# Kernel tuning notes

Measured on AMD Instinct MI355X. Metric: run time of the kernel, lower is better.

The kernel has to match this reference:

```python
import jax, jax.numpy as jnp
import numpy as np

N_NODES = 100000
N_EDGES = 1600000
VOCAB = 50000
F_DIM = 128
N_GRAPHS = 64
N_LABELS = 20


def setup_inputs() -> dict:
    key = jax.random.key(0)
    ks = jax.random.split(key, 12)
    s = 1.0 / np.sqrt(F_DIM)
    inp = {
        "x": jax.random.randint(ks[0], (N_NODES,), 0, VOCAB),
        "edge_index": jax.random.randint(ks[1], (2, N_EDGES), 0, N_NODES),
        "batch": jnp.sort(jax.random.randint(ks[2], (N_NODES,), 0, N_GRAPHS)),
        "emb": jax.random.normal(ks[3], (VOCAB, F_DIM), jnp.float32),
        "w1_rel": jax.random.normal(ks[4], (F_DIM, F_DIM), jnp.float32) * s,
        "w1_root": jax.random.normal(ks[5], (F_DIM, F_DIM), jnp.float32) * s,
        "b1": jnp.zeros((F_DIM,), jnp.float32),
        "w2_rel": jax.random.normal(ks[6], (F_DIM, F_DIM), jnp.float32) * s,
        "w2_root": jax.random.normal(ks[7], (F_DIM, F_DIM), jnp.float32) * s,
        "b2": jnp.zeros((F_DIM,), jnp.float32),
        "lw1": jax.random.normal(ks[8], (2 * F_DIM, 128), jnp.float32) * (1.0 / np.sqrt(2 * F_DIM)),
        "lb1": jnp.zeros((128,), jnp.float32),
        "lw2": jax.random.normal(ks[9], (128, 64), jnp.float32) * (1.0 / np.sqrt(128)),
        "lb2": jnp.zeros((64,), jnp.float32),
        "lw3": jax.random.normal(ks[10], (64, N_LABELS), jnp.float32) * (1.0 / np.sqrt(64)),
        "lb3": jnp.zeros((N_LABELS,), jnp.float32),
    }
    return inp


def graph_conv(h, src, dst, w_rel, w_root, b):
    # PyG GraphConv (aggr='add'): out_i = W_rel @ sum_{j->i} h_j + b + W_root @ h_i
    agg = jax.ops.segment_sum(h[src], dst, num_segments=N_NODES)  # [N, F]
    return agg @ w_rel + b + h @ w_root


def reference(x, edge_index, batch, emb, w1_rel, w1_root, b1,
              w2_rel, w2_root, b2, lw1, lb1, lw2, lb2, lw3, lb3):
    src, dst = edge_index[0], edge_index[1]
    h = emb[x]                                              # [N, F]
    h = jax.nn.relu(graph_conv(h, src, dst, w1_rel, w1_root, b1))
    h = jax.nn.relu(graph_conv(h, src, dst, w2_rel, w2_root, b2))
    # global max pool + global mean pool per graph
    gmax = jax.ops.segment_max(h, batch, num_segments=N_GRAPHS)  # [G, F]
    gsum = jax.ops.segment_sum(h, batch, num_segments=N_GRAPHS)
    counts = jax.ops.segment_sum(jnp.ones((N_NODES,), h.dtype), batch,
                                 num_segments=N_GRAPHS)
    gmean = gsum / jnp.maximum(counts, 1.0)[:, None]
    g = jnp.concatenate([gmax, gmean], axis=1)              # [G, 2F]
    g = jax.nn.relu(g @ lw1 + lb1)
    g = jax.nn.relu(g @ lw2 + lb2)
    # NOTE: original applies log_softmax over dim=0 (the graph dim) - kept faithful
    return jax.nn.log_softmax(g @ lw3 + lb3, axis=0)
```

## Files before the change

### kernel.cpp

```cpp
#include <hip/hip_runtime.h>
#include <hip/hip_bf16.h>

#define N_NODES   100000
#define N_EDGES   1600000
#define N_GRAPHS  64
#define FDIM      128
#define N_LABELS  20
#define NBK       64
#define P_BKT     1563
#define NCHUNKS   64
#define CHUNK     25000
#define SCAN_M    (P_BKT * NCHUNKS)
#define SB_BLOCKS 391
#define APITCH    40
#define PCHUNKS   32

typedef __bf16 bf16x8 __attribute__((ext_vector_type(8)));
typedef float  f32x4  __attribute__((ext_vector_type(4)));
union frag_u { uint4 u; bf16x8 b; };

__device__ __forceinline__ unsigned bfr(float v) {
  unsigned b = __float_as_uint(v);
  return (b + 0x7fffu + ((b >> 16) & 1u)) >> 16;
}

__global__ __launch_bounds__(256) void init_kernel(
    float* __restrict__ pool, float* __restrict__ zrow,
    int* __restrict__ csr, int* __restrict__ csr2, int* __restrict__ offsets) {
  int i = blockIdx.x * 256 + threadIdx.x;
  if (i < N_GRAPHS * 256) pool[i] = 0.f;
  if (i < FDIM) zrow[i] = 0.f;
  if (i < 8) { csr[N_EDGES + i] = 0; csr2[N_EDGES + i] = 0; }
  if (i == 8) offsets[N_NODES] = N_EDGES;
}

__global__ __launch_bounds__(256) void cvt_emb_kernel(
    const float* __restrict__ emb, unsigned short* __restrict__ embbf) {
  int i = blockIdx.x * 256 + threadIdx.x;
  float4 v = ((const float4*)emb)[i];
  uint2 o;
  o.x = bfr(v.x) | (bfr(v.y) << 16);
  o.y = bfr(v.z) | (bfr(v.w) << 16);
  ((uint2*)embbf)[i] = o;
}

__global__ __launch_bounds__(256) void cvt_w_kernel(
    const float* __restrict__ w1rel, const float* __restrict__ w1rt,
    const float* __restrict__ w2rel, const float* __restrict__ w2rt,
    unsigned short* __restrict__ wt1, unsigned short* __restrict__ wt2) {
  int gid = blockIdx.x * 256 + threadIdx.x;
  int l = gid >> 15;
  int rem = gid & 32767;
  int c = rem >> 8, k = rem & 255;
  const float* w = l ? ((k < 128) ? w2rel : w2rt) : ((k < 128) ? w1rel : w1rt);
  float v = w[(size_t)(k & 127) * FDIM + c];
  (l ? wt2 : wt1)[c * 256 + k] = (unsigned short)bfr(v);
}

__global__ __launch_bounds__(256) void histA_kernel(
    const int* __restrict__ ei, int* __restrict__ cntmat) {
  __shared__ int hist[P_BKT];
  int tid = threadIdx.x;
  for (int i = tid; i < P_BKT; i += 256) hist[i] = 0;
  __syncthreads();
  int base = blockIdx.x * CHUNK;
  for (int i = tid; i < CHUNK; i += 256) {
    int d = ei[N_EDGES + base + i];
    atomicAdd(&hist[d >> 6], 1);
  }
  __syncthreads();
  for (int p = tid; p < P_BKT; p += 256)
    cntmat[p * NCHUNKS + blockIdx.x] = hist[p];
}

__global__ __launch_bounds__(256) void scanB1_kernel(
    const int* __restrict__ v, int* __restrict__ part,
    int* __restrict__ bsum) {
  __shared__ int s[256];
  int tid = threadIdx.x;
  int i = blockIdx.x * 256 + tid;
  int val = (i < SCAN_M) ? v[i] : 0;
  s[tid] = val;
  __syncthreads();
  for (int off = 1; off < 256; off <<= 1) {
    int t = (tid >= off) ? s[tid - off] : 0;
    __syncthreads();
    s[tid] += t;
    __syncthreads();
  }
  if (i < SCAN_M) part[i] = s[tid] - val;
  if (tid == 255) bsum[blockIdx.x] = s[255];
}

__global__ __launch_bounds__(512) void scanB2_kernel(int* __restrict__ bsum) {
  __shared__ int s[512];
  int tid = threadIdx.x;
  int v = (tid < SB_BLOCKS) ? bsum[tid] : 0;
  s[tid] = v;
  __syncthreads();
  for (int off = 1; off < 512; off <<= 1) {
    int t = (tid >= off) ? s[tid - off] : 0;
    __syncthreads();
    s[tid] += t;
    __syncthreads();
  }
  if (tid < SB_BLOCKS) bsum[tid] = s[tid] - v;
}

__global__ __launch_bounds__(256) void scanB3_kernel(
    int* __restrict__ part, const int* __restrict__ bsum,
    int* __restrict__ bstart) {
  int i = blockIdx.x * 256 + threadIdx.x;
  if (i < SCAN_M) {
    int o = part[i] + bsum[blockIdx.x];
    part[i] = o;
    if ((i & (NCHUNKS - 1)) == 0) bstart[i >> 6] = o;
  }
  if (blockIdx.x == 0 && threadIdx.x == 0) bstart[P_BKT] = N_EDGES;
}

__global__ __launch_bounds__(256) void scatA_kernel(
    const int* __restrict__ ei, const int* __restrict__ S,
    int* __restrict__ ebuf) {
  __shared__ int rc[P_BKT];
  int tid = threadIdx.x;
  for (int p = tid; p < P_BKT; p += 256)
    rc[p] = S[p * NCHUNKS + blockIdx.x];
  __syncthreads();
  int base = blockIdx.x * CHUNK;
  for (int i = tid; i < CHUNK; i += 256) {
    int s0 = ei[base + i];
    int d0 = ei[N_EDGES + base + i];
    int pos = atomicAdd(&rc[d0 >> 6], 1);
    ebuf[pos] = (s0 << 6) | (d0 & 63);
  }
}

__global__ __launch_bounds__(256) void fill2_kernel(
    const int* __restrict__ ebuf, const int* __restrict__ bstart,
    const int* __restrict__ x, int* __restrict__ offsets,
    int* __restrict__ csr, int* __restrict__ csr2) {
  __shared__ int ldeg[NBK], loffs[NBK], rc2[NBK];
  int tid = threadIdx.x;
  int p = blockIdx.x;
  int beg = bstart[p], end = bstart[p + 1];
  if (tid < NBK) ldeg[tid] = 0;
  __syncthreads();
  for (int i = beg + tid; i < end; i += 256)
    atomicAdd(&ldeg[ebuf[i] & 63], 1);
  __syncthreads();
  if (tid == 0) {
    int run = 0;
    for (int r = 0; r < NBK; ++r) { loffs[r] = run; run += ldeg[r]; }
  }
  __syncthreads();
  if (tid < NBK) {
    rc2[tid] = loffs[tid];
    int gn = p * NBK + tid;
    if (gn < N_NODES) offsets[gn] = beg + loffs[tid];
  }
  __syncthreads();
  for (int i = beg + tid; i < end; i += 256) {
    int e = ebuf[i];
    int ld = e & 63;
    int src = e >> 6;
    int pos = atomicAdd(&rc2[ld], 1);
    csr[beg + pos] = src;
    csr2[beg + pos] = x[src];
  }
}

__global__ __launch_bounds__(256) void agg_kernel(
    const unsigned short* __restrict__ feat, const int* __restrict__ srcidx,
    const int* __restrict__ offs, const float* __restrict__ zrow,
    unsigned short* __restrict__ aggout) {
  int sub = threadIdx.x >> 4;
  int fq  = threadIdx.x & 15;
  int node = blockIdx.x * 16 + sub;

  float4 e0 = make_float4(0.f, 0.f, 0.f, 0.f);
  float4 e1 = make_float4(0.f, 0.f, 0.f, 0.f);
  float4 o0 = make_float4(0.f, 0.f, 0.f, 0.f);
  float4 o1 = make_float4(0.f, 0.f, 0.f, 0.f);
  int s = offs[node], e = offs[node + 1];

  const uint4* __restrict__ fb = (const uint4*)feat;
  const uint4* __restrict__ zb = (const uint4*)zrow;

  int p = s;
  for (; p + 8 <= e; p += 8) {
    const uint4* rp[8];
#pragma unroll
    for (int u = 0; u < 8; ++u)
      rp[u] = fb + (size_t)srcidx[p + u] * 16;
    uint4 w[8];
#pragma unroll
    for (int u = 0; u < 8; ++u) w[u] = rp[u][fq];
#pragma unroll
    for (int u = 0; u < 8; ++u) {
      float4& A = (u & 1) ? o0 : e0;
      float4& B = (u & 1) ? o1 : e1;
      A.x += __uint_as_float(w[u].x << 16);
      A.y += __uint_as_float(w[u].x & 0xffff0000u);
      A.z += __uint_as_float(w[u].y << 16);
      A.w += __uint_as_float(w[u].y & 0xffff0000u);
      B.x += __uint_as_float(w[u].z << 16);
      B.y += __uint_as_float(w[u].z & 0xffff0000u);
      B.z += __uint_as_float(w[u].w << 16);
      B.w += __uint_as_float(w[u].w & 0xffff0000u);
    }
  }
  if (p < e) {
    const uint4* rp[8];
#pragma unroll
    for (int u = 0; u < 8; ++u) {
      int iu = srcidx[p + u];
      rp[u] = (p + u < e) ? (fb + (size_t)iu * 16) : zb;
    }
    uint4 w[8];
#pragma unroll
    for (int u = 0; u < 8; ++u) w[u] = rp[u][fq];
#pragma unroll
    for (int u = 0; u < 8; ++u) {
      float4& A = (u & 1) ? o0 : e0;
      float4& B = (u & 1) ? o1 : e1;
      A.x += __uint_as_float(w[u].x << 16);
      A.y += __uint_as_float(w[u].x & 0xffff0000u);
      A.z += __uint_as_float(w[u].y << 16);
      A.w += __uint_as_float(w[u].y & 0xffff0000u);
      B.x += __uint_as_float(w[u].z << 16);
      B.y += __uint_as_float(w[u].z & 0xffff0000u);
      B.z += __uint_as_float(w[u].w << 16);
      B.w += __uint_as_float(w[u].w & 0xffff0000u);
    }
  }
  float f0 = e0.x + o0.x, f1 = e0.y + o0.y, f2 = e0.z + o0.z, f3 = e0.w + o0.w;
  float f4 = e1.x + o1.x, f5 = e1.y + o1.y, f6 = e1.z + o1.z, f7 = e1.w + o1.w;
  uint4 o;
  o.x = bfr(f0) | (bfr(f1) << 16);
  o.y = bfr(f2) | (bfr(f3) << 16);
  o.z = bfr(f4) | (bfr(f5) << 16);
  o.w = bfr(f6) | (bfr(f7) << 16);
  ((uint4*)aggout)[(size_t)node * 16 + fq] = o;
}

__global__ __launch_bounds__(256) void gemm_kernel(
    const unsigned short* __restrict__ aggbf,
    const unsigned short* __restrict__ rootbf,
    const int* __restrict__ hidx,
    const unsigned short* __restrict__ wt,
    const float* __restrict__ bias,
    float* __restrict__ hout_f32,
    unsigned short* __restrict__ hout_bf) {
  __shared__ unsigned short A_s[128 * APITCH];
  __shared__ unsigned short B_s[128 * APITCH];
  int tid = threadIdx.x;
  int nodeBase = blockIdx.x * 128;
  int lane = tid & 63;
  int wv = tid >> 6;
  int wbase = wv * 32;
  int lo = lane & 15, hi = lane >> 4;

  const unsigned short* a_src[2];
  const unsigned short* r_src[2];
  int s_dst[2], w_off[2];
#pragma unroll
  for (int i = 0; i < 2; ++i) {
    int f = tid + 256 * i;
    int row = f >> 2, part = f & 3;
    int gn = nodeBase + row;
    if (gn > N_NODES - 1) gn = N_NODES - 1;
    int hr = hidx ? hidx[gn] : gn;
    a_src[i] = aggbf + (size_t)gn * FDIM + part * 8;
    r_src[i] = rootbf + (size_t)hr * FDIM + part * 8;
    s_dst[i] = row * APITCH + part * 8;
    w_off[i] = row * 256 + part * 8;
  }

  f32x4 acc[2][8];
#pragma unroll
  for (int nt = 0; nt < 8; ++nt) {
    float b = bias[nt * 16 + lo];
#pragma unroll
    for (int mt = 0; mt < 2; ++mt) {
      acc[mt][nt][0] = b; acc[mt][nt][1] = b;
      acc[mt][nt][2] = b; acc[mt][nt][3] = b;
    }
  }

#pragma unroll 1
  for (int t = 0; t < 8; ++t) {
    __syncthreads();
#pragma unroll
    for (int i = 0; i < 2; ++i) {
      const unsigned short* sa = (t < 4) ? (a_src[i] + t * 32)
                                         : (r_src[i] + (t - 4) * 32);
      *(uint4*)&A_s[s_dst[i]] = *(const uint4*)sa;
      *(uint4*)&B_s[s_dst[i]] = *(const uint4*)(wt + w_off[i] + t * 32);
    }
    __syncthreads();

    frag_u af[2], bfv[8];
#pragma unroll
    for (int mt = 0; mt < 2; ++mt)
      af[mt].u = *(const uint4*)&A_s[(wbase + mt * 16 + lo) * APITCH + hi * 8];
#pragma unroll
    for (int nt = 0; nt < 8; ++nt)
      bfv[nt].u = *(const uint4*)&B_s[(nt * 16 + lo) * APITCH + hi * 8];
#pragma unroll
    for (int mt = 0; mt < 2; ++mt)
#pragma unroll
      for (int nt = 0; nt < 8; ++nt)
        acc[mt][nt] = __builtin_amdgcn_mfma_f32_16x16x32_bf16(
            af[mt].b, bfv[nt].b, acc[mt][nt], 0, 0, 0);
  }

#pragma unroll
  for (int mt = 0; mt < 2; ++mt) {
#pragma unroll
    for (int r = 0; r < 4; ++r) {
      int n = nodeBase + wbase + mt * 16 + hi * 4 + r;
      if (n < N_NODES) {
        if (hout_bf) {
          unsigned short* o = hout_bf + (size_t)n * FDIM + lo;
#pragma unroll
          for (int nt = 0; nt < 8; ++nt)
            o[nt * 16] = (unsigned short)bfr(fmaxf(acc[mt][nt][r], 0.f));
        } else {
          float* o = hout_f32 + (size_t)n * FDIM + lo;
#pragma unroll
          for (int nt = 0; nt < 8; ++nt)
            o[nt * 16] = fmaxf(acc[mt][nt][r], 0.f);
        }
      }
    }
  }
}

__global__ void find_starts_kernel(const int* __restrict__ batch,
                                   int* __restrict__ start) {
  int i = blockIdx.x * 256 + threadIdx.x;
  if (i >= N_NODES) return;
  int b  = batch[i];
  int bp = (i == 0) ? -1 : batch[i - 1];
  for (int g = bp + 1; g <= b; ++g) start[g] = i;
  if (i == N_NODES - 1) {
    for (int g = b + 1; g <= N_GRAPHS; ++g) start[g] = N_NODES;
  }
}

__global__ __launch_bounds__(256) void pool_kernel(
    const float* __restrict__ h2, const int* __restrict__ start,
    float* __restrict__ pool) {
  __shared__ float4 rmax[8][32];
  __shared__ float4 rsum[8][32];
  int g = blockIdx.x >> 5;
  int c = blockIdx.x & (PCHUNKS - 1);
  int tid = threadIdx.x;
  int fq = tid & 31;
  int sub = tid >> 5;
  int s = start[g], e = start[g + 1];
  int len = e - s;
  int lo = s + (int)(((long long)len * c) >> 5);
  int hi = s + (int)(((long long)len * (c + 1)) >> 5);
  float4 mx = make_float4(0.f, 0.f, 0.f, 0.f);
  float4 sm = make_float4(0.f, 0.f, 0.f, 0.f);
  for (int n = lo + sub; n < hi; n += 8) {
    float4 v = ((const float4*)(h2 + (size_t)n * FDIM))[fq];
    mx.x = fmaxf(mx.x, v.x); mx.y = fmaxf(mx.y, v.y);
    mx.z = fmaxf(mx.z, v.z); mx.w = fmaxf(mx.w, v.w);
    sm.x += v.x; sm.y += v.y; sm.z += v.z; sm.w += v.w;
  }
  rmax[sub][fq] = mx;
  rsum[sub][fq] = sm;
  __syncthreads();
  if (sub == 0) {
#pragma unroll
    for (int r = 1; r < 8; ++r) {
      float4 m2 = rmax[r][fq], s2 = rsum[r][fq];
      mx.x = fmaxf(mx.x, m2.x); mx.y = fmaxf(mx.y, m2.y);
      mx.z = fmaxf(mx.z, m2.z); mx.w = fmaxf(mx.w, m2.w);
      sm.x += s2.x; sm.y += s2.y; sm.z += s2.z; sm.w += s2.w;
    }
    unsigned int* pm = (unsigned int*)&pool[g * 256 + fq * 4];
    atomicMax(pm + 0, __float_as_uint(mx.x));
    atomicMax(pm + 1, __float_as_uint(mx.y));
    atomicMax(pm + 2, __float_as_uint(mx.z));
    atomicMax(pm + 3, __float_as_uint(mx.w));
    float* ps = &pool[g * 256 + 128 + fq * 4];
    atomicAdd(ps + 0, sm.x);
    atomicAdd(ps + 1, sm.y);
    atomicAdd(ps + 2, sm.z);
    atomicAdd(ps + 3, sm.w);
  }
}

__global__ void pool_fin_kernel(float* __restrict__ pool,
                                const int* __restrict__ start) {
  int gid = blockIdx.x * 256 + threadIdx.x;
  int g = gid >> 7, f = gid & 127;
  int cnt = start[g + 1] - start[g];
  float c = (float)(cnt > 1 ? cnt : 1);
  pool[g * 256 + 128 + f] /= c;
}

__global__ void head1_kernel(const float* __restrict__ pool,
                             const float* __restrict__ lw1,
                             const float* __restrict__ lb1,
                             float* __restrict__ t1) {
  int gid = blockIdx.x * 256 + threadIdx.x;
  int r = gid >> 7, c = gid & 127;
  float acc = lb1[c];
  for (int k = 0; k < 256; ++k) acc += pool[r * 256 + k] * lw1[k * 128 + c];
  t1[gid] = fmaxf(acc, 0.f);
}

__global__ void head2_kernel(const float* __restrict__ t1,
                             const float* __restrict__ lw2,
                             const float* __restrict__ lb2,
                             float* __restrict__ t2) {
  int gid = blockIdx.x * 256 + threadIdx.x;
  int r = gid >> 6, c = gid & 63;
  float acc = lb2[c];
  for (int k = 0; k < 128; ++k) acc += t1[r * 128 + k] * lw2[k * 64 + c];
  t2[gid] = fmaxf(acc, 0.f);
}

__global__ __launch_bounds__(256) void head3_kernel(
    const float* __restrict__ t2, const float* __restrict__ lw3,
    const float* __restrict__ lb3, float* __restrict__ out) {
  __shared__ float lg[N_GRAPHS * N_LABELS];
  __shared__ float col[N_LABELS];
  int tid = threadIdx.x;
  for (int o = tid; o < N_GRAPHS * N_LABELS; o += 256) {
    int r = o / N_LABELS, c = o - r * N_LABELS;
    float acc = lb3[c];
    for (int k = 0; k < 64; ++k) acc += t2[r * 64 + k] * lw3[k * N_LABELS + c];
    lg[o] = acc;
  }
  __syncthreads();
  if (tid < N_LABELS) {
    float m = -1e30f;
    for (int r = 0; r < N_GRAPHS; ++r) m = fmaxf(m, lg[r * N_LABELS + tid]);
    float s = 0.f;
    for (int r = 0; r < N_GRAPHS; ++r) s += expf(lg[r * N_LABELS + tid] - m);
    col[tid] = m + logf(s);
  }
  __syncthreads();
  for (int o = tid; o < N_GRAPHS * N_LABELS; o += 256) {
    int c = o % N_LABELS;
    out[o] = lg[o] - col[c];
  }
}

extern "C" void kernel_launch(void* const* d_in, const int* in_sizes, int n_in,
                              void* d_out, int out_size, void* d_ws, size_t ws_size,
                              hipStream_t stream) {
  const int*   x     = (const int*)  d_in[0];
  const int*   ei    = (const int*)  d_in[1];
  const int*   batch = (const int*)  d_in[2];
  const float* emb   = (const float*)d_in[3];
  const float* w1rel = (const float*)d_in[4];
  const float* w1rt  = (const float*)d_in[5];
  const float* b1    = (const float*)d_in[6];
  const float* w2rel = (const float*)d_in[7];
  const float* w2rt  = (const float*)d_in[8];
  const float* b2    = (const float*)d_in[9];
  const float* lw1   = (const float*)d_in[10];
  const float* lb1   = (const float*)d_in[11];
  const float* lw2   = (const float*)d_in[12];
  const float* lb2   = (const float*)d_in[13];
  const float* lw3   = (const float*)d_in[14];
  const float* lb3   = (const float*)d_in[15];
  float* out = (float*)d_out;

  char* ws = (char*)d_ws;
  const size_t HB   = 51200000;
  const size_t CSRB = 6400128;
  const size_t OFFB = 400128;
  float* hB      = (float*)(ws);
  unsigned short* embbf = (unsigned short*)(ws);
  unsigned short* aggbf = (unsigned short*)(ws + HB);
  int*   ebuf    = (int*)  (ws + HB);
  int*   csr     = (int*)  (ws + 2 * HB);
  int*   cntmat  = (int*)  (ws + 2 * HB);
  int*   S       = (int*)  (ws + 2 * HB + 400128);
  int*   bsum    = (int*)  (ws + 2 * HB + 800256);
  int*   csr2    = (int*)  (ws + 2 * HB + CSRB);
  int*   offsets = (int*)  (ws + 2 * HB + 2 * CSRB);
  int*   bstart  = (int*)  (ws + 2 * HB + 2 * CSRB + OFFB);
  float* zrow    = (float*)(ws + 2 * HB + 2 * CSRB + OFFB + 6400);
  int*   start   = (int*)  (ws + 2 * HB + 2 * CSRB + OFFB + 6912);
  float* pool    = (float*)(ws + 2 * HB + 2 * CSRB + OFFB + 7424);
  float* t1      = (float*)(ws + 2 * HB + 2 * CSRB + OFFB + 72960);
  float* t2      = (float*)(ws + 2 * HB + 2 * CSRB + OFFB + 105728);
  unsigned short* hbf =
      (unsigned short*)(ws + 2 * HB + 2 * CSRB + OFFB + 122112);
  unsigned short* wt1 =
      (unsigned short*)(ws + 2 * HB + 2 * CSRB + OFFB + 122112 + 25600000);
  unsigned short* wt2 = wt1 + 128 * 256;

  init_kernel<<<64, 256, 0, stream>>>(pool, zrow, csr, csr2, offsets);

  cvt_emb_kernel<<<6250, 256, 0, stream>>>(emb, embbf);
  cvt_w_kernel<<<256, 256, 0, stream>>>(w1rel, w1rt, w2rel, w2rt, wt1, wt2);

  histA_kernel<<<NCHUNKS, 256, 0, stream>>>(ei, cntmat);
  scanB1_kernel<<<SB_BLOCKS, 256, 0, stream>>>(cntmat, S, bsum);
  scanB2_kernel<<<1, 512, 0, stream>>>(bsum);
  scanB3_kernel<<<SB_BLOCKS, 256, 0, stream>>>(S, bsum, bstart);
  scatA_kernel<<<NCHUNKS, 256, 0, stream>>>(ei, S, ebuf);
  fill2_kernel<<<P_BKT, 256, 0, stream>>>(ebuf, bstart, x, offsets, csr, csr2);

  agg_kernel<<<N_NODES / 16, 256, 0, stream>>>(embbf, csr2, offsets, zrow, aggbf);
  gemm_kernel<<<(N_NODES + 127) / 128, 256, 0, stream>>>(
      aggbf, embbf, x, wt1, b1, (float*)nullptr, hbf);

  agg_kernel<<<N_NODES / 16, 256, 0, stream>>>(hbf, csr, offsets, zrow, aggbf);
  gemm_kernel<<<(N_NODES + 127) / 128, 256, 0, stream>>>(
      aggbf, hbf, (const int*)nullptr, wt2, b2, hB,
      (unsigned short*)nullptr);

  find_starts_kernel<<<SB_BLOCKS, 256, 0, stream>>>(batch, start);
  pool_kernel<<<N_GRAPHS * PCHUNKS, 256, 0, stream>>>(hB, start, pool);
  pool_fin_kernel<<<32, 256, 0, stream>>>(pool, start);

  head1_kernel<<<32, 256, 0, stream>>>(pool, lw1, lb1, t1);
  head2_kernel<<<16, 256, 0, stream>>>(t1, lw2, lb2, t2);
  head3_kernel<<<1, 256, 0, stream>>>(t2, lw3, lb3, out);
}
```

Before: 425.5 us.

## Split edge bucketing into 512 chunks and unroll aggregation gather to 16

```diff
diff --git a/kernel.cpp b/kernel.cpp
--- a/kernel.cpp
+++ b/kernel.cpp
@@ -8,9 +8,11 @@
 #define N_LABELS  20
 #define NBK       64
 #define P_BKT     1563
-#define NCHUNKS   64
-#define CHUNK     25000
+#define NCHUNKS   512
+#define NCHUNKS_LOG 9
+#define CHUNK     3125
 #define SCAN_M    (P_BKT * NCHUNKS)
+#define SB1_BLOCKS 3126
 #define SB_BLOCKS 391
 #define APITCH    40
 #define PCHUNKS   32
@@ -95,8 +97,15 @@
 __global__ __launch_bounds__(512) void scanB2_kernel(int* __restrict__ bsum) {
   __shared__ int s[512];
   int tid = threadIdx.x;
-  int v = (tid < SB_BLOCKS) ? bsum[tid] : 0;
-  s[tid] = v;
+  int v[8];
+  int tot = 0;
+#pragma unroll
+  for (int j = 0; j < 8; ++j) {
+    int idx = tid * 8 + j;
+    v[j] = (idx < SB1_BLOCKS) ? bsum[idx] : 0;
+    tot += v[j];
+  }
+  s[tid] = tot;
   __syncthreads();
   for (int off = 1; off < 512; off <<= 1) {
     int t = (tid >= off) ? s[tid - off] : 0;
@@ -104,7 +113,14 @@
     s[tid] += t;
     __syncthreads();
   }
-  if (tid < SB_BLOCKS) bsum[tid] = s[tid] - v;
+  int run = s[tid] - tot;
+#pragma unroll
+  for (int j = 0; j < 8; ++j) {
+    int idx = tid * 8 + j;
+    int val = v[j];
+    if (idx < SB1_BLOCKS) bsum[idx] = run;
+    run += val;
+  }
 }
 
 __global__ __launch_bounds__(256) void scanB3_kernel(
@@ -114,7 +130,7 @@
   if (i < SCAN_M) {
     int o = part[i] + bsum[blockIdx.x];
     part[i] = o;
-    if ((i & (NCHUNKS - 1)) == 0) bstart[i >> 6] = o;
+    if ((i & (NCHUNKS - 1)) == 0) bstart[i >> NCHUNKS_LOG] = o;
   }
   if (blockIdx.x == 0 && threadIdx.x == 0) bstart[P_BKT] = N_EDGES;
 }
@@ -170,6 +186,20 @@
   }
 }
 
+#define ACC8(WV)                                           \
+  {                                                        \
+    float4& A = ((WV)&1) ? o0 : e0;                        \
+    float4& B = ((WV)&1) ? o1 : e1;                        \
+    A.x += __uint_as_float(w[WV].x << 16);                 \
+    A.y += __uint_as_float(w[WV].x & 0xffff0000u);         \
+    A.z += __uint_as_float(w[WV].y << 16);                 \
+    A.w += __uint_as_float(w[WV].y & 0xffff0000u);         \
+    B.x += __uint_as_float(w[WV].z << 16);                 \
+    B.y += __uint_as_float(w[WV].z & 0xffff0000u);         \
+    B.z += __uint_as_float(w[WV].w << 16);                 \
+    B.w += __uint_as_float(w[WV].w & 0xffff0000u);         \
+  }
+
 __global__ __launch_bounds__(256) void agg_kernel(
     const unsigned short* __restrict__ feat, const int* __restrict__ srcidx,
     const int* __restrict__ offs, const float* __restrict__ zrow,
@@ -188,6 +218,17 @@
   const uint4* __restrict__ zb = (const uint4*)zrow;
 
   int p = s;
+  for (; p + 16 <= e; p += 16) {
+    const uint4* rp[16];
+#pragma unroll
+    for (int u = 0; u < 16; ++u)
+      rp[u] = fb + (size_t)srcidx[p + u] * 16;
+    uint4 w[16];
+#pragma unroll
+    for (int u = 0; u < 16; ++u) w[u] = rp[u][fq];
+    ACC8(0) ACC8(1) ACC8(2) ACC8(3) ACC8(4) ACC8(5) ACC8(6) ACC8(7)
+    ACC8(8) ACC8(9) ACC8(10) ACC8(11) ACC8(12) ACC8(13) ACC8(14) ACC8(15)
+  }
   for (; p + 8 <= e; p += 8) {
     const uint4* rp[8];
 #pragma unroll
@@ -196,19 +237,7 @@
     uint4 w[8];
 #pragma unroll
     for (int u = 0; u < 8; ++u) w[u] = rp[u][fq];
-#pragma unroll
-    for (int u = 0; u < 8; ++u) {
-      float4& A = (u & 1) ? o0 : e0;
-      float4& B = (u & 1) ? o1 : e1;
-      A.x += __uint_as_float(w[u].x << 16);
-      A.y += __uint_as_float(w[u].x & 0xffff0000u);
-      A.z += __uint_as_float(w[u].y << 16);
-      A.w += __uint_as_float(w[u].y & 0xffff0000u);
-      B.x += __uint_as_float(w[u].z << 16);
-      B.y += __uint_as_float(w[u].z & 0xffff0000u);
-      B.z += __uint_as_float(w[u].w << 16);
-      B.w += __uint_as_float(w[u].w & 0xffff0000u);
-    }
+    ACC8(0) ACC8(1) ACC8(2) ACC8(3) ACC8(4) ACC8(5) ACC8(6) ACC8(7)
   }
   if (p < e) {
     const uint4* rp[8];
@@ -220,19 +249,7 @@
     uint4 w[8];
 #pragma unroll
     for (int u = 0; u < 8; ++u) w[u] = rp[u][fq];
-#pragma unroll
-    for (int u = 0; u < 8; ++u) {
-      float4& A = (u & 1) ? o0 : e0;
-      float4& B = (u & 1) ? o1 : e1;
-      A.x += __uint_as_float(w[u].x << 16);
-      A.y += __uint_as_float(w[u].x & 0xffff0000u);
-      A.z += __uint_as_float(w[u].y << 16);
-      A.w += __uint_as_float(w[u].y & 0xffff0000u);
-      B.x += __uint_as_float(w[u].z << 16);
-      B.y += __uint_as_float(w[u].z & 0xffff0000u);
-      B.z += __uint_as_float(w[u].w << 16);
-      B.w += __uint_as_float(w[u].w & 0xffff0000u);
-    }
+    ACC8(0) ACC8(1) ACC8(2) ACC8(3) ACC8(4) ACC8(5) ACC8(6) ACC8(7)
   }
   float f0 = e0.x + o0.x, f1 = e0.y + o0.y, f2 = e0.z + o0.z, f3 = e0.w + o0.w;
   float f4 = e1.x + o1.x, f5 = e1.y + o1.y, f6 = e1.z + o1.z, f7 = e1.w + o1.w;
@@ -480,12 +497,12 @@
   const size_t OFFB = 400128;
   float* hB      = (float*)(ws);
   unsigned short* embbf = (unsigned short*)(ws);
+  int*   cntmat  = (int*)  (ws + 13000000);
+  int*   S       = (int*)  (ws + 16500000);
+  int*   bsum    = (int*)  (ws + 20000000);
   unsigned short* aggbf = (unsigned short*)(ws + HB);
   int*   ebuf    = (int*)  (ws + HB);
   int*   csr     = (int*)  (ws + 2 * HB);
-  int*   cntmat  = (int*)  (ws + 2 * HB);
-  int*   S       = (int*)  (ws + 2 * HB + 400128);
-  int*   bsum    = (int*)  (ws + 2 * HB + 800256);
   int*   csr2    = (int*)  (ws + 2 * HB + CSRB);
   int*   offsets = (int*)  (ws + 2 * HB + 2 * CSRB);
   int*   bstart  = (int*)  (ws + 2 * HB + 2 * CSRB + OFFB);
@@ -506,9 +523,9 @@
   cvt_w_kernel<<<256, 256, 0, stream>>>(w1rel, w1rt, w2rel, w2rt, wt1, wt2);
 
   histA_kernel<<<NCHUNKS, 256, 0, stream>>>(ei, cntmat);
-  scanB1_kernel<<<SB_BLOCKS, 256, 0, stream>>>(cntmat, S, bsum);
+  scanB1_kernel<<<SB1_BLOCKS, 256, 0, stream>>>(cntmat, S, bsum);
   scanB2_kernel<<<1, 512, 0, stream>>>(bsum);
-  scanB3_kernel<<<SB_BLOCKS, 256, 0, stream>>>(S, bsum, bstart);
+  scanB3_kernel<<<SB1_BLOCKS, 256, 0, stream>>>(S, bsum, bstart);
   scatA_kernel<<<NCHUNKS, 256, 0, stream>>>(ei, S, ebuf);
   fill2_kernel<<<P_BKT, 256, 0, stream>>>(ebuf, bstart, x, offsets, csr, csr2);
 
```

Measured after the change: 392.6 us. -7.7%, faster.

## Split edge bucketing into more chunks and keep GEMM A fragments in registers

Applied to the files above, without the earlier changes.

```diff
diff --git a/kernel.cpp b/kernel.cpp
--- a/kernel.cpp
+++ b/kernel.cpp
@@ -8,11 +8,13 @@
 #define N_LABELS  20
 #define NBK       64
 #define P_BKT     1563
-#define NCHUNKS   64
-#define CHUNK     25000
+#define NCHUNKS   512
+#define NCHUNKS_LOG 9
+#define CHUNK     3125
 #define SCAN_M    (P_BKT * NCHUNKS)
+#define SB1_BLOCKS 3126
 #define SB_BLOCKS 391
-#define APITCH    40
+#define BPITCH    136
 #define PCHUNKS   32
 
 typedef __bf16 bf16x8 __attribute__((ext_vector_type(8)));
@@ -30,8 +32,8 @@
   int i = blockIdx.x * 256 + threadIdx.x;
   if (i < N_GRAPHS * 256) pool[i] = 0.f;
   if (i < FDIM) zrow[i] = 0.f;
-  if (i < 8) { csr[N_EDGES + i] = 0; csr2[N_EDGES + i] = 0; }
-  if (i == 8) offsets[N_NODES] = N_EDGES;
+  if (i < 16) { csr[N_EDGES + i] = 0; csr2[N_EDGES + i] = 0; }
+  if (i == 16) offsets[N_NODES] = N_EDGES;
 }
 
 __global__ __launch_bounds__(256) void cvt_emb_kernel(
@@ -95,8 +97,15 @@
 __global__ __launch_bounds__(512) void scanB2_kernel(int* __restrict__ bsum) {
   __shared__ int s[512];
   int tid = threadIdx.x;
-  int v = (tid < SB_BLOCKS) ? bsum[tid] : 0;
-  s[tid] = v;
+  int v[8];
+  int tot = 0;
+#pragma unroll
+  for (int j = 0; j < 8; ++j) {
+    int idx = tid * 8 + j;
+    v[j] = (idx < SB1_BLOCKS) ? bsum[idx] : 0;
+    tot += v[j];
+  }
+  s[tid] = tot;
   __syncthreads();
   for (int off = 1; off < 512; off <<= 1) {
     int t = (tid >= off) ? s[tid - off] : 0;
@@ -104,7 +113,14 @@
     s[tid] += t;
     __syncthreads();
   }
-  if (tid < SB_BLOCKS) bsum[tid] = s[tid] - v;
+  int run = s[tid] - tot;
+#pragma unroll
+  for (int j = 0; j < 8; ++j) {
+    int idx = tid * 8 + j;
+    int val = v[j];
+    if (idx < SB1_BLOCKS) bsum[idx] = run;
+    run += val;
+  }
 }
 
 __global__ __launch_bounds__(256) void scanB3_kernel(
@@ -114,7 +130,7 @@
   if (i < SCAN_M) {
     int o = part[i] + bsum[blockIdx.x];
     part[i] = o;
-    if ((i & (NCHUNKS - 1)) == 0) bstart[i >> 6] = o;
+    if ((i & (NCHUNKS - 1)) == 0) bstart[i >> NCHUNKS_LOG] = o;
   }
   if (blockIdx.x == 0 && threadIdx.x == 0) bstart[P_BKT] = N_EDGES;
 }
@@ -244,7 +260,7 @@
   ((uint4*)aggout)[(size_t)node * 16 + fq] = o;
 }
 
-__global__ __launch_bounds__(256) void gemm_kernel(
+__global__ __launch_bounds__(256, 2) void gemm_kernel(
     const unsigned short* __restrict__ aggbf,
     const unsigned short* __restrict__ rootbf,
     const int* __restrict__ hidx,
@@ -252,8 +268,7 @@
     const float* __restrict__ bias,
     float* __restrict__ hout_f32,
     unsigned short* __restrict__ hout_bf) {
-  __shared__ unsigned short A_s[128 * APITCH];
-  __shared__ unsigned short B_s[128 * APITCH];
+  __shared__ unsigned short B_s[128 * BPITCH];
   int tid = threadIdx.x;
   int nodeBase = blockIdx.x * 128;
   int lane = tid & 63;
@@ -261,20 +276,26 @@
   int wbase = wv * 32;
   int lo = lane & 15, hi = lane >> 4;
 
-  const unsigned short* a_src[2];
-  const unsigned short* r_src[2];
-  int s_dst[2], w_off[2];
-#pragma unroll
-  for (int i = 0; i < 2; ++i) {
-    int f = tid + 256 * i;
-    int row = f >> 2, part = f & 3;
-    int gn = nodeBase + row;
-    if (gn > N_NODES - 1) gn = N_NODES - 1;
-    int hr = hidx ? hidx[gn] : gn;
-    a_src[i] = aggbf + (size_t)gn * FDIM + part * 8;
-    r_src[i] = rootbf + (size_t)hr * FDIM + part * 8;
-    s_dst[i] = row * APITCH + part * 8;
-    w_off[i] = row * 256 + part * 8;
+  int gnode[2], hroot[2];
+#pragma unroll
+  for (int mt = 0; mt < 2; ++mt) {
+    int g = nodeBase + wbase + mt * 16 + lo;
+    if (g > N_NODES - 1) g = N_NODES - 1;
+    gnode[mt] = g;
+    hroot[mt] = hidx ? hidx[g] : g;
+  }
+
+  frag_u afr[2][8];
+#pragma unroll
+  for (int mt = 0; mt < 2; ++mt) {
+#pragma unroll
+    for (int t = 0; t < 4; ++t)
+      afr[mt][t].u =
+          *(const uint4*)(aggbf + (size_t)gnode[mt] * FDIM + t * 32 + hi * 8);
+#pragma unroll
+    for (int t = 0; t < 4; ++t)
+      afr[mt][4 + t].u =
+          *(const uint4*)(rootbf + (size_t)hroot[mt] * FDIM + t * 32 + hi * 8);
   }
 
   f32x4 acc[2][8];
@@ -288,31 +309,31 @@
     }
   }
 
-#pragma unroll 1
-  for (int t = 0; t < 8; ++t) {
+  int sr = tid >> 1;
+  int so = (tid & 1) * 64;
+
+#pragma unroll
+  for (int h = 0; h < 2; ++h) {
     __syncthreads();
 #pragma unroll
-    for (int i = 0; i < 2; ++i) {
-      const unsigned short* sa = (t < 4) ? (a_src[i] + t * 32)
-                                         : (r_src[i] + (t - 4) * 32);
-      *(uint4*)&A_s[s_dst[i]] = *(const uint4*)sa;
-      *(uint4*)&B_s[s_dst[i]] = *(const uint4*)(wt + w_off[i] + t * 32);
-    }
+    for (int i = 0; i < 8; ++i)
+      *(uint4*)(B_s + sr * BPITCH + so + i * 8) =
+          *(const uint4*)(wt + sr * 256 + h * 128 + so + i * 8);
     __syncthreads();
-
-    frag_u af[2], bfv[8];
-#pragma unroll
-    for (int mt = 0; mt < 2; ++mt)
-      af[mt].u = *(const uint4*)&A_s[(wbase + mt * 16 + lo) * APITCH + hi * 8];
-#pragma unroll
-    for (int nt = 0; nt < 8; ++nt)
-      bfv[nt].u = *(const uint4*)&B_s[(nt * 16 + lo) * APITCH + hi * 8];
-#pragma unroll
-    for (int mt = 0; mt < 2; ++mt)
+#pragma unroll
+    for (int tt = 0; tt < 4; ++tt) {
+      frag_u bfv[8];
 #pragma unroll
       for (int nt = 0; nt < 8; ++nt)
-        acc[mt][nt] = __builtin_amdgcn_mfma_f32_16x16x32_bf16(
-            af[mt].b, bfv[nt].b, acc[mt][nt], 0, 0, 0);
+        bfv[nt].u =
+            *(const uint4*)&B_s[(nt * 16 + lo) * BPITCH + tt * 32 + hi * 8];
+#pragma unroll
+      for (int mt = 0; mt < 2; ++mt)
+#pragma unroll
+        for (int nt = 0; nt < 8; ++nt)
+          acc[mt][nt] = __builtin_amdgcn_mfma_f32_16x16x32_bf16(
+              afr[mt][h * 4 + tt].b, bfv[nt].b, acc[mt][nt], 0, 0, 0);
+    }
   }
 
 #pragma unroll
@@ -480,12 +501,12 @@
   const size_t OFFB = 400128;
   float* hB      = (float*)(ws);
   unsigned short* embbf = (unsigned short*)(ws);
+  int*   cntmat  = (int*)  (ws + 13000000);
+  int*   S       = (int*)  (ws + 16500000);
+  int*   bsum    = (int*)  (ws + 20000000);
   unsigned short* aggbf = (unsigned short*)(ws + HB);
   int*   ebuf    = (int*)  (ws + HB);
   int*   csr     = (int*)  (ws + 2 * HB);
-  int*   cntmat  = (int*)  (ws + 2 * HB);
-  int*   S       = (int*)  (ws + 2 * HB + 400128);
-  int*   bsum    = (int*)  (ws + 2 * HB + 800256);
   int*   csr2    = (int*)  (ws + 2 * HB + CSRB);
   int*   offsets = (int*)  (ws + 2 * HB + 2 * CSRB);
   int*   bstart  = (int*)  (ws + 2 * HB + 2 * CSRB + OFFB);
@@ -506,9 +527,9 @@
   cvt_w_kernel<<<256, 256, 0, stream>>>(w1rel, w1rt, w2rel, w2rt, wt1, wt2);
 
   histA_kernel<<<NCHUNKS, 256, 0, stream>>>(ei, cntmat);
-  scanB1_kernel<<<SB_BLOCKS, 256, 0, stream>>>(cntmat, S, bsum);
+  scanB1_kernel<<<SB1_BLOCKS, 256, 0, stream>>>(cntmat, S, bsum);
   scanB2_kernel<<<1, 512, 0, stream>>>(bsum);
-  scanB3_kernel<<<SB_BLOCKS, 256, 0, stream>>>(S, bsum, bstart);
+  scanB3_kernel<<<SB1_BLOCKS, 256, 0, stream>>>(S, bsum, bstart);
   scatA_kernel<<<NCHUNKS, 256, 0, stream>>>(ei, S, ebuf);
   fill2_kernel<<<P_BKT, 256, 0, stream>>>(ebuf, bstart, x, offsets, csr, csr2);
 
```

New measurement: 380.4 us. -10.6%, faster.
